# Performance work log

Hardware: AMD Instinct MI355X
Metric: run time of the kernel (lower is better)

Reference implementation:

```python
import jax, jax.numpy as jnp
import numpy as np

N = 50000      # nodes
E = 800000     # edges (before self-loops)
DIN = 256      # in_channel
H = 1          # heads (PyG GATConv default)
C = 128        # out_channel per head
NEG_SLOPE = 0.2


def setup_inputs() -> dict:
    key = jax.random.key(0)
    k1, k2, k3, k4, k5 = jax.random.split(key, 5)
    x = jax.random.normal(k1, (N, DIN), jnp.float32)
    # random edges guaranteed to have no self-loops (PyG removes then re-adds them)
    src = jax.random.randint(k2, (E,), 0, N, dtype=jnp.int32)
    off = jax.random.randint(k3, (E,), 1, N, dtype=jnp.int32)
    dst = (src + off) % N
    edge_index = jnp.stack([src, dst])  # [2, E], row0=source j, row1=target i
    W = jax.random.normal(k4, (DIN, H * C), jnp.float32) / np.sqrt(DIN)
    att = jax.random.normal(k5, (1, H, 2 * C), jnp.float32) * 0.1
    bias = jnp.zeros((H * C,), jnp.float32)
    return {"x": x, "edge_index": edge_index, "W": W, "att": att, "bias": bias}


def reference(x, edge_index, W, att, bias):
    n = x.shape[0]
    h = (x @ W).reshape(n, H, C)                       # [N,H,C]
    # add self-loops (PyG GATConv forward)
    loops = jnp.arange(n, dtype=edge_index.dtype)
    src = jnp.concatenate([edge_index[0], loops])       # [Et]
    dst = jnp.concatenate([edge_index[1], loops])       # [Et]
    h_i = h[dst]                                        # [Et,H,C] target feats
    h_j = h[src]                                        # [Et,H,C] source feats
    # per-edge attention logit: sum(cat(x_i, x_j) * att)
    alpha = jnp.sum(jnp.concatenate([h_i, h_j], axis=-1) * att, axis=-1)  # [Et,H]
    alpha = jax.nn.leaky_relu(alpha, NEG_SLOPE)
    # segment softmax grouped by destination node (numerically stable)
    amax = jax.ops.segment_max(alpha, dst, num_segments=n)  # [N,H]
    ex = jnp.exp(alpha - amax[dst])
    denom = jax.ops.segment_sum(ex, dst, num_segments=n)    # [N,H]
    a = ex / (denom[dst] + 1e-16)                            # [Et,H]
    # scatter-aggregate weighted source features to targets
    out = jax.ops.segment_sum(h_j * a[..., None], dst, num_segments=n)  # [N,H,C]
    return out.reshape(n, H * C) + bias
```

## Files before the change

### kernel.cpp

```cpp
#include <hip/hip_runtime.h>
#include <hip/hip_bf16.h>

constexpr int N_NODES = 50000;
constexpr int DIN     = 256;
constexpr int C_OUT   = 128;
constexpr int E_EDGES = 800000;
constexpr int ET      = E_EDGES + N_NODES;
constexpr float NEG_SLOPE = 0.2f;

constexpr int NHI     = 196;
constexpr int NCHUNK  = 416;
constexpr int EPC     = 2048;
constexpr int TOTCNT  = NHI * NCHUNK;
constexpr int NSB     = (TOTCNT + 2047) / 2048;
constexpr int WCONV_BLOCKS = (DIN * C_OUT) / 256;
constexpr int GEMM_RPB     = 64;
constexpr int GEMM_BLOCKS  = (N_NODES + GEMM_RPB - 1) / GEMM_RPB;
constexpr int AGG_NPB      = 32;
constexpr int AGG_BLOCKS   = (N_NODES + AGG_NPB - 1) / AGG_NPB;

typedef __attribute__((ext_vector_type(8))) short short8v;
typedef __attribute__((ext_vector_type(4))) float f32x4;

static __device__ __forceinline__ ushort f2bf(float f) {
    __hip_bfloat16 b = __float2bfloat16(f);
    return *reinterpret_cast<ushort*>(&b);
}
static __device__ __forceinline__ short f2bfs(float f) {
    __hip_bfloat16 b = __float2bfloat16(f);
    return *reinterpret_cast<short*>(&b);
}

__global__ __launch_bounds__(256) void count_wconv(const float* __restrict__ W,
                                                   const int* __restrict__ ei,
                                                   ushort* __restrict__ wt,
                                                   int* __restrict__ cnt) {
    __shared__ int hist[NHI];
    const int t = threadIdx.x;
    if (blockIdx.x < NCHUNK) {
        const int c = blockIdx.x;
        if (t < NHI) hist[t] = 0;
        __syncthreads();
        #pragma unroll
        for (int i = 0; i < 8; i++) {
            const int e = c * EPC + i * 256 + t;
            if (e < ET) {
                const int d = (e < E_EDGES) ? ei[E_EDGES + e] : (e - E_EDGES);
                atomicAdd(&hist[d >> 8], 1);
            }
        }
        __syncthreads();
        if (t < NHI) cnt[t * NCHUNK + c] = hist[t];
        return;
    }
    const int idx = (blockIdx.x - NCHUNK) * 256 + t;
    if (idx < DIN * C_OUT) {
        const int k = idx >> 7, col = idx & 127;
        const int ks = k >> 5, kgrp = (k >> 3) & 3, j = k & 7;
        const int cc = col >> 4, col16 = col & 15;
        wt[((ks * 8 + cc) * 64 + kgrp * 16 + col16) * 8 + j] = f2bf(W[idx]);
    }
}

__global__ __launch_bounds__(256) void gemm_scan1(const float* __restrict__ x,
                                                  const ushort* __restrict__ wt,
                                                  const float* __restrict__ att,
                                                  const int* __restrict__ cnt,
                                                  int* __restrict__ bsum,
                                                  ushort* __restrict__ hb,
                                                  float* __restrict__ s_dst,
                                                  float* __restrict__ s_src) {
    __shared__ ushort lw[DIN * C_OUT / 2];
    __shared__ int wsum[4];
    const int t = threadIdx.x;

    if (blockIdx.x < NSB) {
        const int b = blockIdx.x;
        const int i0 = b * 2048 + t * 8;
        int s = 0;
        #pragma unroll
        for (int j = 0; j < 8; j++) { const int i = i0 + j; if (i < TOTCNT) s += cnt[i]; }
        #pragma unroll
        for (int off = 32; off; off >>= 1) s += __shfl_xor(s, off);
        if ((t & 63) == 0) wsum[t >> 6] = s;
        __syncthreads();
        if (t == 0) bsum[b] = wsum[0] + wsum[1] + wsum[2] + wsum[3];
        return;
    }

    const int gb = blockIdx.x - NSB;
    const int lane = t & 63, wv = t >> 6;
    const int col16 = lane & 15, kgrp = lane >> 4;
    const int rowbase = gb * GEMM_RPB + wv * 16;
    int r0 = rowbase + col16; if (r0 >= N_NODES) r0 = N_NODES - 1;
    const float* xr0 = x + (size_t)r0 * DIN + kgrp * 8;

    f32x4 acc[8] = {};
    const short8v* lwf = (const short8v*)lw;
    #pragma unroll
    for (int ph = 0; ph < 2; ph++) {
        if (ph) __syncthreads();
        {
            const uint4* src = (const uint4*)(wt + ph * (DIN * C_OUT / 2));
            uint4* dst = (uint4*)lw;
            #pragma unroll
            for (int i = 0; i < 8; i++) dst[t + i * 256] = src[t + i * 256];
        }
        short8v A0[4];
        #pragma unroll
        for (int ks = 0; ks < 4; ks++) {
            const int kg = ph * 4 + ks;
            const float4 v0 = *(const float4*)(xr0 + kg * 32);
            const float4 v1 = *(const float4*)(xr0 + kg * 32 + 4);
            short8v a;
            a[0] = f2bfs(v0.x); a[1] = f2bfs(v0.y); a[2] = f2bfs(v0.z); a[3] = f2bfs(v0.w);
            a[4] = f2bfs(v1.x); a[5] = f2bfs(v1.y); a[6] = f2bfs(v1.z); a[7] = f2bfs(v1.w);
            A0[ks] = a;
        }
        __syncthreads();
        #pragma unroll
        for (int ks = 0; ks < 4; ks++) {
            #pragma unroll
            for (int c = 0; c < 8; c++) {
                const short8v bfr = lwf[(ks * 8 + c) * 64 + lane];
                acc[c] = __builtin_amdgcn_mfma_f32_16x16x32_bf16(A0[ks], bfr, acc[c], 0, 0, 0);
            }
        }
    }

    float attd[8], atts[8];
    #pragma unroll
    for (int c = 0; c < 8; c++) {
        attd[c] = att[c * 16 + col16];
        atts[c] = att[C_OUT + c * 16 + col16];
    }
    #pragma unroll
    for (int j = 0; j < 4; j++) {
        const int row = rowbase + kgrp * 4 + j;
        const bool ok = (row < N_NODES);
        float pd = 0.f, ps = 0.f;
        #pragma unroll
        for (int c = 0; c < 8; c++) {
            const float hv = acc[c][j];
            pd += hv * attd[c];
            ps += hv * atts[c];
            if (ok) hb[(size_t)row * C_OUT + c * 16 + col16] = f2bf(hv);
        }
        #pragma unroll
        for (int off = 1; off < 16; off <<= 1) {
            pd += __shfl_xor(pd, off);
            ps += __shfl_xor(ps, off);
        }
        if (col16 == 0 && ok) { s_dst[row] = pd; s_src[row] = ps; }
    }
}

__global__ void scan_mid(const int* __restrict__ bsum, int* __restrict__ bbase) {
    const int lane = threadIdx.x;
    const int v = (lane < NSB) ? bsum[lane] : 0;
    int x = v;
    #pragma unroll
    for (int off = 1; off < 64; off <<= 1) {
        const int y = __shfl_up(x, off);
        if (lane >= off) x += y;
    }
    if (lane < NSB) bbase[lane] = x - v;
}

__global__ __launch_bounds__(256) void scan_fin(int* __restrict__ cnt,
                                                const int* __restrict__ bbase) {
    __shared__ int wsum[4];
    const int t = threadIdx.x, b = blockIdx.x;
    const int lane = t & 63, wv = t >> 6;
    const int i0 = b * 2048 + t * 8;
    int c[8]; int ts = 0;
    #pragma unroll
    for (int j = 0; j < 8; j++) {
        const int i = i0 + j;
        c[j] = (i < TOTCNT) ? cnt[i] : 0;
        ts += c[j];
    }
    int x = ts;
    #pragma unroll
    for (int off = 1; off < 64; off <<= 1) {
        const int y = __shfl_up(x, off);
        if (lane >= off) x += y;
    }
    if (lane == 63) wsum[wv] = x;
    __syncthreads();
    int wbase = 0;
    #pragma unroll
    for (int w = 0; w < 4; w++) if (w < wv) wbase += wsum[w];
    int base = bbase[b] + wbase + (x - ts);
    #pragma unroll
    for (int j = 0; j < 8; j++) {
        const int i = i0 + j;
        if (i < TOTCNT) cnt[i] = base;
        base += c[j];
    }
}

__global__ __launch_bounds__(256) void part_kernel(const int* __restrict__ ei,
                                                   const int* __restrict__ sco,
                                                   int2* __restrict__ ebuf) {
    __shared__ int basel[NHI];
    __shared__ int curl[NHI];
    const int t = threadIdx.x, c = blockIdx.x;
    if (t < NHI) { basel[t] = sco[t * NCHUNK + c]; curl[t] = 0; }
    __syncthreads();
    #pragma unroll
    for (int i = 0; i < 8; i++) {
        const int e = c * EPC + i * 256 + t;
        if (e < ET) {
            int s, d;
            if (e < E_EDGES) { s = ei[e]; d = ei[E_EDGES + e]; }
            else             { s = e - E_EDGES; d = s; }
            const int hi = d >> 8;
            const int r = atomicAdd(&curl[hi], 1);
            ebuf[basel[hi] + r] = make_int2(s, d);
        }
    }
}

__global__ __launch_bounds__(256) void final_kernel(const int* __restrict__ sco,
                                                    const int2* __restrict__ ebuf,
                                                    int* __restrict__ offsets,
                                                    int* __restrict__ esrc) {
    __shared__ int histl[256], sA[256], sE[256], curl[256];
    const int t = threadIdx.x, hi = blockIdx.x;
    const int segbase = sco[hi * NCHUNK];
    const int segend  = (hi == NHI - 1) ? ET : sco[(hi + 1) * NCHUNK];
    histl[t] = 0;
    if (hi == 0 && t == 0) offsets[N_NODES] = ET;
    __syncthreads();
    for (int k = segbase + t; k < segend; k += 256)
        atomicAdd(&histl[ebuf[k].y & 255], 1);
    __syncthreads();
    const int v = histl[t];
    sA[t] = v;
    __syncthreads();
    #pragma unroll
    for (int off = 1; off < 256; off <<= 1) {
        const int y = (t >= off) ? sA[t - off] : 0;
        __syncthreads();
        sA[t] += y;
        __syncthreads();
    }
    sE[t] = sA[t] - v;
    curl[t] = 0;
    const int node = hi * 256 + t;
    if (node < N_NODES) offsets[node] = segbase + sE[t];
    __syncthreads();
    for (int k = segbase + t; k < segend; k += 256) {
        const int2 e2 = ebuf[k];
        const int lo = e2.y & 255;
        const int r = atomicAdd(&curl[lo], 1);
        esrc[segbase + sE[lo] + r] = e2.x;
    }
}

__global__ __launch_bounds__(256) void aggregate_kernel(
    const ushort* __restrict__ hb, const int* __restrict__ offsets,
    const int* __restrict__ esrc, const float* __restrict__ s_dst,
    const float* __restrict__ s_src, const float* __restrict__ bias,
    float* __restrict__ out) {
    const int t = threadIdx.x;
    const int wv = t >> 6, lane = t & 63;
    const int sub = lane >> 3, l8 = lane & 7;
    const int node = blockIdx.x * AGG_NPB + wv * 8 + sub;
    const bool valid = (node < N_NODES);

    const int beg = valid ? offsets[node] : 0;
    const int end = valid ? offsets[node + 1] : 0;
    const float sd = valid ? s_dst[node] : 0.f;
    float den = 0.f;
    float acc[16] = {};
    const uint4* __restrict__ h4 = (const uint4*)hb;

    for (int e = beg; e < end; e++) {
        const int s = esrc[e];
        float a = sd + s_src[s];
        a = (a > 0.f) ? a : NEG_SLOPE * a;
        const float w = __expf(a);
        den += w;
        const uint4 hv0 = h4[(size_t)s * 16 + l8];
        const uint4 hv1 = h4[(size_t)s * 16 + 8 + l8];
        acc[0]  += w * __uint_as_float(hv0.x << 16);
        acc[1]  += w * __uint_as_float(hv0.x & 0xffff0000u);
        acc[2]  += w * __uint_as_float(hv0.y << 16);
        acc[3]  += w * __uint_as_float(hv0.y & 0xffff0000u);
        acc[4]  += w * __uint_as_float(hv0.z << 16);
        acc[5]  += w * __uint_as_float(hv0.z & 0xffff0000u);
        acc[6]  += w * __uint_as_float(hv0.w << 16);
        acc[7]  += w * __uint_as_float(hv0.w & 0xffff0000u);
        acc[8]  += w * __uint_as_float(hv1.x << 16);
        acc[9]  += w * __uint_as_float(hv1.x & 0xffff0000u);
        acc[10] += w * __uint_as_float(hv1.y << 16);
        acc[11] += w * __uint_as_float(hv1.y & 0xffff0000u);
        acc[12] += w * __uint_as_float(hv1.z << 16);
        acc[13] += w * __uint_as_float(hv1.z & 0xffff0000u);
        acc[14] += w * __uint_as_float(hv1.w << 16);
        acc[15] += w * __uint_as_float(hv1.w & 0xffff0000u);
    }
    if (!valid) return;
    const float inv = 1.f / (den + 1e-16f);
    float* op = out + (size_t)node * C_OUT;
    #pragma unroll
    for (int half = 0; half < 2; half++) {
        const int base = half * 64 + l8 * 8;
        const float4 b0 = *(const float4*)(bias + base);
        const float4 b1 = *(const float4*)(bias + base + 4);
        float4 o0 = make_float4(acc[half * 8 + 0] * inv + b0.x, acc[half * 8 + 1] * inv + b0.y,
                                acc[half * 8 + 2] * inv + b0.z, acc[half * 8 + 3] * inv + b0.w);
        float4 o1 = make_float4(acc[half * 8 + 4] * inv + b1.x, acc[half * 8 + 5] * inv + b1.y,
                                acc[half * 8 + 6] * inv + b1.z, acc[half * 8 + 7] * inv + b1.w);
        *(float4*)(op + base)     = o0;
        *(float4*)(op + base + 4) = o1;
    }
}

extern "C" void kernel_launch(void* const* d_in, const int* in_sizes, int n_in,
                              void* d_out, int out_size, void* d_ws, size_t ws_size,
                              hipStream_t stream) {
    const float* x    = (const float*)d_in[0];
    const int*   ei   = (const int*)d_in[1];
    const float* W    = (const float*)d_in[2];
    const float* att  = (const float*)d_in[3];
    const float* bias = (const float*)d_in[4];
    float* out = (float*)d_out;

    ushort* wt      = (ushort*)d_ws;
    ushort* hbuf    = wt + DIN * C_OUT;
    int2*   ebuf    = (int2*)(hbuf + (size_t)N_NODES * C_OUT);
    float*  s_src   = (float*)(ebuf + ET);
    float*  s_dst   = s_src + N_NODES;
    int*    offsets = (int*)(s_dst + N_NODES);
    int*    esrc    = offsets + N_NODES + 2;
    int*    cnt     = esrc + ET;
    int*    bsum    = cnt + TOTCNT;
    int*    bbase   = bsum + 64;

    count_wconv<<<NCHUNK + WCONV_BLOCKS, 256, 0, stream>>>(W, ei, wt, cnt);
    gemm_scan1<<<NSB + GEMM_BLOCKS, 256, 0, stream>>>(x, wt, att, cnt, bsum,
                                                      hbuf, s_dst, s_src);
    scan_mid<<<1, 64, 0, stream>>>(bsum, bbase);
    scan_fin<<<NSB, 256, 0, stream>>>(cnt, bbase);
    part_kernel<<<NCHUNK, 256, 0, stream>>>(ei, cnt, ebuf);
    final_kernel<<<NHI, 256, 0, stream>>>(cnt, ebuf, offsets, esrc);
    aggregate_kernel<<<AGG_BLOCKS, 256, 0, stream>>>(
        hbuf, offsets, esrc, s_dst, s_src, bias, out);
}
```

Baseline: 88.27 us.

## Fold the three-pass counter scan into one block of the GEMM kernel

Replaces the three-stage exclusive prefix scan (block reduce inside the GEMM launch, a mid scan kernel, a final scan kernel) with a single block that scans all ~81k counters sequentially in 2048-element tiles, running alongside the GEMM blocks. This removes two kernel launches and their serialization gaps. In exchange, one block performs about 40 serial tile iterations, which could become the tail of the GEMM launch if it runs longer than the GEMM work. The esrc offset padding also changes, which keeps int4 alignment for later buffers.

```diff
diff --git a/kernel.cpp b/kernel.cpp
--- a/kernel.cpp
+++ b/kernel.cpp
@@ -12,7 +12,6 @@
 constexpr int NCHUNK  = 416;
 constexpr int EPC     = 2048;
 constexpr int TOTCNT  = NHI * NCHUNK;
-constexpr int NSB     = (TOTCNT + 2047) / 2048;
 constexpr int WCONV_BLOCKS = (DIN * C_OUT) / 256;
 constexpr int GEMM_RPB     = 64;
 constexpr int GEMM_BLOCKS  = (N_NODES + GEMM_RPB - 1) / GEMM_RPB;
@@ -62,33 +61,64 @@
     }
 }
 
-__global__ __launch_bounds__(256) void gemm_scan1(const float* __restrict__ x,
-                                                  const ushort* __restrict__ wt,
-                                                  const float* __restrict__ att,
-                                                  const int* __restrict__ cnt,
-                                                  int* __restrict__ bsum,
-                                                  ushort* __restrict__ hb,
-                                                  float* __restrict__ s_dst,
-                                                  float* __restrict__ s_src) {
+__global__ __launch_bounds__(256) void scan_gemm(const float* __restrict__ x,
+                                                 const ushort* __restrict__ wt,
+                                                 const float* __restrict__ att,
+                                                 int* __restrict__ cnt,
+                                                 ushort* __restrict__ hb,
+                                                 float* __restrict__ s_dst,
+                                                 float* __restrict__ s_src) {
     __shared__ ushort lw[DIN * C_OUT / 2];
-    __shared__ int wsum[4];
     const int t = threadIdx.x;
 
-    if (blockIdx.x < NSB) {
-        const int b = blockIdx.x;
-        const int i0 = b * 2048 + t * 8;
-        int s = 0;
-        #pragma unroll
-        for (int j = 0; j < 8; j++) { const int i = i0 + j; if (i < TOTCNT) s += cnt[i]; }
-        #pragma unroll
-        for (int off = 32; off; off >>= 1) s += __shfl_xor(s, off);
-        if ((t & 63) == 0) wsum[t >> 6] = s;
-        __syncthreads();
-        if (t == 0) bsum[b] = wsum[0] + wsum[1] + wsum[2] + wsum[3];
+    if (blockIdx.x == 0) {
+        __shared__ int wsum[4];
+        __shared__ int s_tot[1];
+        const int lane = t & 63, wv = t >> 6;
+        int running = 0;
+        for (int tile = 0; tile < TOTCNT; tile += 2048) {
+            const int i0 = tile + t * 8;
+            int c[8]; int ts = 0;
+            if (i0 + 8 <= TOTCNT) {
+                const int4 a = *(const int4*)(cnt + i0);
+                const int4 b = *(const int4*)(cnt + i0 + 4);
+                c[0]=a.x; c[1]=a.y; c[2]=a.z; c[3]=a.w;
+                c[4]=b.x; c[5]=b.y; c[6]=b.z; c[7]=b.w;
+            } else {
+                #pragma unroll
+                for (int j = 0; j < 8; j++) c[j] = (i0 + j < TOTCNT) ? cnt[i0 + j] : 0;
+            }
+            #pragma unroll
+            for (int j = 0; j < 8; j++) ts += c[j];
+            int xv = ts;
+            #pragma unroll
+            for (int off = 1; off < 64; off <<= 1) {
+                const int y = __shfl_up(xv, off);
+                if (lane >= off) xv += y;
+            }
+            if (lane == 63) wsum[wv] = xv;
+            __syncthreads();
+            int wbase = 0, tot = 0;
+            #pragma unroll
+            for (int w = 0; w < 4; w++) {
+                const int val = wsum[w];
+                if (w < wv) wbase += val;
+                tot += val;
+            }
+            int base = running + wbase + (xv - ts);
+            #pragma unroll
+            for (int j = 0; j < 8; j++) {
+                const int i = i0 + j;
+                if (i < TOTCNT) cnt[i] = base;
+                base += c[j];
+            }
+            running += tot;
+            __syncthreads();
+        }
         return;
     }
 
-    const int gb = blockIdx.x - NSB;
+    const int gb = blockIdx.x - 1;
     const int lane = t & 63, wv = t >> 6;
     const int col16 = lane & 15, kgrp = lane >> 4;
     const int rowbase = gb * GEMM_RPB + wv * 16;
@@ -152,51 +182,6 @@
             ps += __shfl_xor(ps, off);
         }
         if (col16 == 0 && ok) { s_dst[row] = pd; s_src[row] = ps; }
-    }
-}
-
-__global__ void scan_mid(const int* __restrict__ bsum, int* __restrict__ bbase) {
-    const int lane = threadIdx.x;
-    const int v = (lane < NSB) ? bsum[lane] : 0;
-    int x = v;
-    #pragma unroll
-    for (int off = 1; off < 64; off <<= 1) {
-        const int y = __shfl_up(x, off);
-        if (lane >= off) x += y;
-    }
-    if (lane < NSB) bbase[lane] = x - v;
-}
-
-__global__ __launch_bounds__(256) void scan_fin(int* __restrict__ cnt,
-                                                const int* __restrict__ bbase) {
-    __shared__ int wsum[4];
-    const int t = threadIdx.x, b = blockIdx.x;
-    const int lane = t & 63, wv = t >> 6;
-    const int i0 = b * 2048 + t * 8;
-    int c[8]; int ts = 0;
-    #pragma unroll
-    for (int j = 0; j < 8; j++) {
-        const int i = i0 + j;
-        c[j] = (i < TOTCNT) ? cnt[i] : 0;
-        ts += c[j];
-    }
-    int x = ts;
-    #pragma unroll
-    for (int off = 1; off < 64; off <<= 1) {
-        const int y = __shfl_up(x, off);
-        if (lane >= off) x += y;
-    }
-    if (lane == 63) wsum[wv] = x;
-    __syncthreads();
-    int wbase = 0;
-    #pragma unroll
-    for (int w = 0; w < 4; w++) if (w < wv) wbase += wsum[w];
-    int base = bbase[b] + wbase + (x - ts);
-    #pragma unroll
-    for (int j = 0; j < 8; j++) {
-        const int i = i0 + j;
-        if (i < TOTCNT) cnt[i] = base;
-        base += c[j];
     }
 }
 
@@ -335,16 +320,12 @@
     float*  s_src   = (float*)(ebuf + ET);
     float*  s_dst   = s_src + N_NODES;
     int*    offsets = (int*)(s_dst + N_NODES);
-    int*    esrc    = offsets + N_NODES + 2;
+    int*    esrc    = offsets + N_NODES + 4;
     int*    cnt     = esrc + ET;
-    int*    bsum    = cnt + TOTCNT;
-    int*    bbase   = bsum + 64;
 
     count_wconv<<<NCHUNK + WCONV_BLOCKS, 256, 0, stream>>>(W, ei, wt, cnt);
-    gemm_scan1<<<NSB + GEMM_BLOCKS, 256, 0, stream>>>(x, wt, att, cnt, bsum,
-                                                      hbuf, s_dst, s_src);
-    scan_mid<<<1, 64, 0, stream>>>(bsum, bbase);
-    scan_fin<<<NSB, 256, 0, stream>>>(cnt, bbase);
+    scan_gemm<<<1 + GEMM_BLOCKS, 256, 0, stream>>>(x, wt, att, cnt,
+                                                   hbuf, s_dst, s_src);
     part_kernel<<<NCHUNK, 256, 0, stream>>>(ei, cnt, ebuf);
     final_kernel<<<NHI, 256, 0, stream>>>(cnt, ebuf, offsets, esrc);
     aggregate_kernel<<<AGG_BLOCKS, 256, 0, stream>>>(
```

New measurement: 132.2 us. 1.5x slower.
